# Kernel tuning notes

Measured on AMD Instinct MI355X. Metric: run time of the kernel, lower is better.

The kernel has to match this reference:

```python
import jax, jax.numpy as jnp
import numpy as np

# Gemma config constants (layer_idx=0 -> 'sliding_attention')
H = 8          # num query heads
KVH = 4        # num kv heads
DH = 256       # head_dim
SW = 1024      # sliding_window
ROPE_BASE = 10000.0   # rope_local_base_freq (sliding layer)
EPS = 1e-6
SCALE = 256.0 ** -0.5  # query_pre_attn_scalar ** -0.5


def _rms_norm(x, w):
    # Gemma RMSNorm: fp32 norm, scale by (1 + w)
    x32 = x.astype(jnp.float32)
    n = x32 * jax.lax.rsqrt(jnp.mean(x32 * x32, axis=-1, keepdims=True) + EPS)
    return (n * (1.0 + w.astype(jnp.float32))).astype(x.dtype)


def _rope_cos_sin(S):
    inv_freq = 1.0 / (ROPE_BASE ** (jnp.arange(0, DH, 2, dtype=jnp.float32) / DH))
    freqs = jnp.outer(jnp.arange(S, dtype=jnp.float32), inv_freq)  # [S, DH/2]
    emb = jnp.concatenate([freqs, freqs], axis=-1)                 # [S, DH]
    return jnp.cos(emb), jnp.sin(emb)


def _rotate_half(x):
    x1, x2 = jnp.split(x, 2, axis=-1)
    return jnp.concatenate([-x2, x1], axis=-1)


def _apply_rope(x, cos, sin):
    # x: [B, H, S, DH]; cos/sin: [S, DH]
    return x * cos[None, None] + _rotate_half(x) * sin[None, None]


def setup_inputs() -> dict:
    key = jax.random.key(0)
    ks = jax.random.split(key, 7)
    B, S, D = 2, 2048, 2048
    w = lambda k, shape: jax.random.normal(k, shape, jnp.float32) * 0.02
    return {
        "hidden_states": jax.random.normal(ks[0], (B, S, D), jnp.float32),
        "Wq": w(ks[1], (H * DH, D)),
        "Wk": w(ks[2], (KVH * DH, D)),
        "Wv": w(ks[3], (KVH * DH, D)),
        "Wo": w(ks[4], (D, H * DH)),
        "q_norm_w": jnp.zeros((DH,), jnp.float32),
        "k_norm_w": jnp.zeros((DH,), jnp.float32),
    }


def reference(hidden_states, Wq, Wk, Wv, Wo, q_norm_w, k_norm_w):
    B, S, D = hidden_states.shape
    # projections (no bias)
    q = jnp.einsum("bsd,ed->bse", hidden_states, Wq).reshape(B, S, H, DH).transpose(0, 2, 1, 3)
    k = jnp.einsum("bsd,ed->bse", hidden_states, Wk).reshape(B, S, KVH, DH).transpose(0, 2, 1, 3)
    v = jnp.einsum("bsd,ed->bse", hidden_states, Wv).reshape(B, S, KVH, DH).transpose(0, 2, 1, 3)
    # Gemma q/k RMSNorm over head_dim, then RoPE (local base for sliding layer)
    q = _rms_norm(q, q_norm_w)
    k = _rms_norm(k, k_norm_w)
    cos, sin = _rope_cos_sin(S)
    q = _apply_rope(q, cos, sin)
    k = _apply_rope(k, cos, sin)
    # GQA: repeat kv heads
    rep = H // KVH
    k = jnp.repeat(k, rep, axis=1)
    v = jnp.repeat(v, rep, axis=1)
    # causal sliding-window mask
    i = jnp.arange(S)[:, None]
    j = jnp.arange(S)[None, :]
    mask = (j <= i) & (i - j < SW)  # [S, S]
    scores = jnp.einsum("bhqd,bhkd->bhqk", q, k) * SCALE
    scores = jnp.where(mask[None, None], scores, jnp.finfo(jnp.float32).min)
    attn = jax.nn.softmax(scores.astype(jnp.float32), axis=-1).astype(q.dtype)
    out = jnp.einsum("bhqk,bhkd->bhqd", attn, v)  # [B, H, S, DH]
    out = out.transpose(0, 2, 1, 3).reshape(B, S, H * DH)
    return jnp.einsum("bse,de->bsd", out, Wo)
```

## Files before the change

### kernel.cpp

```cpp
#include <hip/hip_runtime.h>
#include <hip/hip_bf16.h>


typedef __bf16 bf16x8 __attribute__((ext_vector_type(8)));
typedef __bf16 bf16x4 __attribute__((ext_vector_type(4)));
typedef float f32x4 __attribute__((ext_vector_type(4)));

#define NB 2
#define SEQ 2048
#define DMODEL 2048
#define NH 8
#define NKV 4
#define DHEAD 256
#define SWIN 1024

#define AS1 __attribute__((address_space(1)))
#define AS3 __attribute__((address_space(3)))

static __device__ __forceinline__ void gload_lds16(const void* g, void* l) {
    __builtin_amdgcn_global_load_lds((const AS1 void*)g, (AS3 void*)l, 16, 0, 0);
}

static __device__ __forceinline__ bf16x4 tr16(const __bf16* p) {
    bf16x4 r;
    asm volatile("ds_read_b64_tr_b16 %0, %1" : "=v"(r) : "v"((const AS3 __bf16*)p));
    return r;
}

__global__ void cvt_rope(const float* __restrict__ s0, const float* __restrict__ s1,
                         const float* __restrict__ s2, const float* __restrict__ s3,
                         const float* __restrict__ s4, __bf16* __restrict__ d0,
                         __bf16* __restrict__ d1, __bf16* __restrict__ d2,
                         __bf16* __restrict__ d3, __bf16* __restrict__ d4,
                         float* __restrict__ cosT, float* __restrict__ sinT) {
    if (blockIdx.x >= 20480) {
        int idx = (blockIdx.x - 20480) * 256 + threadIdx.x;
        int s = idx >> 7, i = idx & 127;
        float fr = (float)s * __expf(-(float)i * 0.0719557843f);
        cosT[idx] = cosf(fr);
        sinT[idx] = sinf(fr);
        return;
    }
    int i = blockIdx.x * 256 + threadIdx.x;
    const float* src; __bf16* dst;
    if (i < 2097152) { src = s0; dst = d0; }
    else if (i < 3145728) { i -= 2097152; src = s1; dst = d1; }
    else if (i < 3670016) { i -= 3145728; src = s2; dst = d2; }
    else if (i < 4194304) { i -= 3670016; src = s3; dst = d3; }
    else                  { i -= 4194304; src = s4; dst = d4; }
    f32x4 v = ((const f32x4*)src)[i];
    bf16x4 o;
#pragma unroll
    for (int j = 0; j < 4; ++j) o[j] = (__bf16)v[j];
    ((bf16x4*)dst)[i] = o;
}

template <int OUTBF16>
__global__ __launch_bounds__(512, 2)
void gemm_bt8(const __bf16* __restrict__ A, const __bf16* __restrict__ B,
              void* __restrict__ Cv, int M, int N, int K, int nbx) {
    __shared__ __align__(16) __bf16 sA[2][256 * 64];
    __shared__ __align__(16) __bf16 sB[2][256 * 64];
    const int tid = threadIdx.x;
    const int wave = tid >> 6, lane = tid & 63;
    const int lo = lane & 15, hi = lane >> 4;
    const int wm = wave >> 2, wn = wave & 3;
    const int qq = (int)gridDim.x >> 3;
    const int swz = ((int)blockIdx.x & 7) * qq + ((int)blockIdx.x >> 3);
    const int bx = swz % nbx, by = swz / nbx;
    const int brow = by * 256, bcol = bx * 256;
    const int xr = lo & 7;

    int aoff[4];
#pragma unroll
    for (int i = 0; i < 4; ++i) {
        int n = i * 512 + tid, r = n >> 3, s = n & 7;
        aoff[i] = r * K + ((s ^ (r & 7)) << 3);
    }
    const __bf16* Ab = A + (size_t)brow * K;
    const __bf16* Bb = B + (size_t)bcol * K;

    auto stgA = [&](int bsel, int kt, int h) {
        const __bf16* ga = Ab + kt * 64;
#pragma unroll
        for (int ii = 0; ii < 2; ++ii) {
            int i = h + ii * 2;
            gload_lds16(ga + aoff[i], (char*)&sA[bsel][0] + (i * 512 + wave * 64) * 16);
        }
    };
    auto stgB = [&](int bsel, int kt, int h) {
        const __bf16* gb = Bb + kt * 64;
#pragma unroll
        for (int i = 2 * h; i < 2 * h + 2; ++i)
            gload_lds16(gb + aoff[i], (char*)&sB[bsel][0] + (i * 512 + wave * 64) * 16);
    };

    f32x4 acc[8][4] = {};
    const int nt = K >> 6;

    stgA(0, 0, 0); stgA(0, 0, 1); stgB(0, 0, 0); stgB(0, 0, 1);
    stgA(1, 1, 0); stgA(1, 1, 1); stgB(1, 1, 0); stgB(1, 1, 1);
    asm volatile("s_waitcnt vmcnt(8)" ::: "memory");
    __builtin_amdgcn_s_barrier();

    for (int t = 0; t < nt; ++t) {
        const int buf = t & 1;
        const bool pre = (t + 2 < nt);
        const __bf16* sa = &sA[buf][0];
        const __bf16* sb = &sB[buf][0];
        bf16x8 af[8], b0[4], b1[4];
#pragma unroll
        for (int m = 0; m < 4; ++m)
#pragma unroll
            for (int ks = 0; ks < 2; ++ks)
                af[m * 2 + ks] = *(const bf16x8*)&sa[(wm * 128 + m * 16 + lo) * 64 + (((ks * 4 + hi) ^ xr) << 3)];
#pragma unroll
        for (int n = 0; n < 2; ++n)
#pragma unroll
            for (int ks = 0; ks < 2; ++ks)
                b0[n * 2 + ks] = *(const bf16x8*)&sb[(wn * 64 + n * 16 + lo) * 64 + (((ks * 4 + hi) ^ xr) << 3)];
        __builtin_amdgcn_sched_barrier(0);
        __builtin_amdgcn_s_barrier();
        __builtin_amdgcn_s_setprio(1);
#pragma unroll
        for (int m = 0; m < 4; ++m)
#pragma unroll
            for (int n = 0; n < 2; ++n)
#pragma unroll
                for (int ks = 0; ks < 2; ++ks)
                    acc[m][n] = __builtin_amdgcn_mfma_f32_16x16x32_bf16(af[m * 2 + ks], b0[n * 2 + ks], acc[m][n], 0, 0, 0);
        __builtin_amdgcn_s_setprio(0);
        __builtin_amdgcn_sched_barrier(0);
        __builtin_amdgcn_s_barrier();
#pragma unroll
        for (int n = 0; n < 2; ++n)
#pragma unroll
            for (int ks = 0; ks < 2; ++ks)
                b1[n * 2 + ks] = *(const bf16x8*)&sb[(wn * 64 + (n + 2) * 16 + lo) * 64 + (((ks * 4 + hi) ^ xr) << 3)];
        if (pre) stgA(buf, t + 2, 0);
        __builtin_amdgcn_sched_barrier(0);
        __builtin_amdgcn_s_barrier();
        __builtin_amdgcn_s_setprio(1);
#pragma unroll
        for (int m = 0; m < 4; ++m)
#pragma unroll
            for (int n = 0; n < 2; ++n)
#pragma unroll
                for (int ks = 0; ks < 2; ++ks)
                    acc[m][n + 2] = __builtin_amdgcn_mfma_f32_16x16x32_bf16(af[m * 2 + ks], b1[n * 2 + ks], acc[m][n + 2], 0, 0, 0);
        __builtin_amdgcn_s_setprio(0);
        __builtin_amdgcn_sched_barrier(0);
        __builtin_amdgcn_s_barrier();
#pragma unroll
        for (int m = 0; m < 4; ++m)
#pragma unroll
            for (int ks = 0; ks < 2; ++ks)
                af[m * 2 + ks] = *(const bf16x8*)&sa[(wm * 128 + (m + 4) * 16 + lo) * 64 + (((ks * 4 + hi) ^ xr) << 3)];
        if (pre) stgB(buf, t + 2, 1);
        __builtin_amdgcn_sched_barrier(0);
        __builtin_amdgcn_s_barrier();
        __builtin_amdgcn_s_setprio(1);
#pragma unroll
        for (int m = 0; m < 4; ++m)
#pragma unroll
            for (int n = 0; n < 2; ++n)
#pragma unroll
                for (int ks = 0; ks < 2; ++ks)
                    acc[m + 4][n + 2] = __builtin_amdgcn_mfma_f32_16x16x32_bf16(af[m * 2 + ks], b1[n * 2 + ks], acc[m + 4][n + 2], 0, 0, 0);
        __builtin_amdgcn_s_setprio(0);
        __builtin_amdgcn_sched_barrier(0);
        __builtin_amdgcn_s_barrier();
        if (pre) { stgA(buf, t + 2, 1); stgB(buf, t + 2, 0); }
        __builtin_amdgcn_sched_barrier(0);
        __builtin_amdgcn_s_setprio(1);
#pragma unroll
        for (int m = 0; m < 4; ++m)
#pragma unroll
            for (int n = 0; n < 2; ++n)
#pragma unroll
                for (int ks = 0; ks < 2; ++ks)
                    acc[m + 4][n] = __builtin_amdgcn_mfma_f32_16x16x32_bf16(af[m * 2 + ks], b0[n * 2 + ks], acc[m + 4][n], 0, 0, 0);
        __builtin_amdgcn_s_setprio(0);
        if (pre) asm volatile("s_waitcnt vmcnt(8)" ::: "memory");
        else     asm volatile("s_waitcnt vmcnt(0)" ::: "memory");
        __builtin_amdgcn_sched_barrier(0);
        __builtin_amdgcn_s_barrier();
    }

#pragma unroll
    for (int m = 0; m < 8; ++m) {
        int row = brow + wm * 128 + m * 16 + hi * 4;
#pragma unroll
        for (int n = 0; n < 4; ++n) {
            int col = bcol + wn * 64 + n * 16 + lo;
            if constexpr (OUTBF16) {
                __bf16* cp = (__bf16*)Cv + (size_t)row * N + col;
#pragma unroll
                for (int j = 0; j < 4; ++j)
                    cp[(size_t)j * N] = (__bf16)acc[m][n][j];
            } else {
                float* cp = (float*)Cv + (size_t)row * N + col;
#pragma unroll
                for (int j = 0; j < 4; ++j)
                    cp[(size_t)j * N] = acc[m][n][j];
            }
        }
    }
}

__global__ __launch_bounds__(512, 2)
void gemm_bt8n(const __bf16* __restrict__ A, const __bf16* __restrict__ B,
               float* __restrict__ C, int M, int N, int K, int nbx) {
    __shared__ __align__(16) __bf16 sA[2][256 * 64];
    __shared__ __align__(16) __bf16 sB[2][128 * 64];
    const int tid = threadIdx.x;
    const int wave = tid >> 6, lane = tid & 63;
    const int lo = lane & 15, hi = lane >> 4;
    const int wm = wave >> 1, wn = wave & 1;
    const int qq = (int)gridDim.x >> 3;
    const int swz = ((int)blockIdx.x & 7) * qq + ((int)blockIdx.x >> 3);
    const int bx = swz % nbx, by = swz / nbx;
    const int brow = by * 256, bcol = bx * 128;
    const int xr = lo & 7;

    int aoff[4], boff[2];
#pragma unroll
    for (int i = 0; i < 4; ++i) {
        int n = i * 512 + tid, r = n >> 3, s = n & 7;
        aoff[i] = r * K + ((s ^ (r & 7)) << 3);
    }
#pragma unroll
    for (int i = 0; i < 2; ++i) {
        int n = i * 512 + tid, r = n >> 3, s = n & 7;
        boff[i] = r * K + ((s ^ (r & 7)) << 3);
    }
    const __bf16* Ab = A + (size_t)brow * K;
    const __bf16* Bb = B + (size_t)bcol * K;

    auto stgAall = [&](int bsel, int kt) {
        const __bf16* ga = Ab + kt * 64;
#pragma unroll
        for (int i = 0; i < 4; ++i)
            gload_lds16(ga + aoff[i], (char*)&sA[bsel][0] + (i * 512 + wave * 64) * 16);
    };
    auto stgBall = [&](int bsel, int kt) {
        const __bf16* gb = Bb + kt * 64;
#pragma unroll
        for (int i = 0; i < 2; ++i)
            gload_lds16(gb + boff[i], (char*)&sB[bsel][0] + (i * 512 + wave * 64) * 16);
    };

    f32x4 acc[4][4] = {};
    const int nt = K >> 6;

    stgAall(0, 0); stgBall(0, 0);
    stgAall(1, 1); stgBall(1, 1);
    asm volatile("s_waitcnt vmcnt(6)" ::: "memory");
    __builtin_amdgcn_s_barrier();

    for (int t = 0; t < nt; ++t) {
        const int buf = t & 1;
        const bool pre = (t + 2 < nt);
        const __bf16* sa = &sA[buf][0];
        const __bf16* sb = &sB[buf][0];
        bf16x8 af[4], b0[4], b1[4];
#pragma unroll
        for (int m = 0; m < 2; ++m)
#pragma unroll
            for (int ks = 0; ks < 2; ++ks)
                af[m * 2 + ks] = *(const bf16x8*)&sa[(wm * 64 + m * 16 + lo) * 64 + (((ks * 4 + hi) ^ xr) << 3)];
#pragma unroll
        for (int n = 0; n < 2; ++n)
#pragma unroll
            for (int ks = 0; ks < 2; ++ks)
                b0[n * 2 + ks] = *(const bf16x8*)&sb[(wn * 64 + n * 16 + lo) * 64 + (((ks * 4 + hi) ^ xr) << 3)];
        __builtin_amdgcn_sched_barrier(0);
        __builtin_amdgcn_s_barrier();
        __builtin_amdgcn_s_setprio(1);
#pragma unroll
        for (int m = 0; m < 2; ++m)
#pragma unroll
            for (int n = 0; n < 2; ++n)
#pragma unroll
                for (int ks = 0; ks < 2; ++ks)
                    acc[m][n] = __builtin_amdgcn_mfma_f32_16x16x32_bf16(af[m * 2 + ks], b0[n * 2 + ks], acc[m][n], 0, 0, 0);
        __builtin_amdgcn_s_setprio(0);
        __builtin_amdgcn_sched_barrier(0);
        __builtin_amdgcn_s_barrier();
#pragma unroll
        for (int n = 0; n < 2; ++n)
#pragma unroll
            for (int ks = 0; ks < 2; ++ks)
                b1[n * 2 + ks] = *(const bf16x8*)&sb[(wn * 64 + (n + 2) * 16 + lo) * 64 + (((ks * 4 + hi) ^ xr) << 3)];
        __builtin_amdgcn_sched_barrier(0);
        __builtin_amdgcn_s_barrier();
        __builtin_amdgcn_s_setprio(1);
#pragma unroll
        for (int m = 0; m < 2; ++m)
#pragma unroll
            for (int n = 0; n < 2; ++n)
#pragma unroll
                for (int ks = 0; ks < 2; ++ks)
                    acc[m][n + 2] = __builtin_amdgcn_mfma_f32_16x16x32_bf16(af[m * 2 + ks], b1[n * 2 + ks], acc[m][n + 2], 0, 0, 0);
        __builtin_amdgcn_s_setprio(0);
        __builtin_amdgcn_sched_barrier(0);
        __builtin_amdgcn_s_barrier();
#pragma unroll
        for (int m = 0; m < 2; ++m)
#pragma unroll
            for (int ks = 0; ks < 2; ++ks)
                af[m * 2 + ks] = *(const bf16x8*)&sa[(wm * 64 + (m + 2) * 16 + lo) * 64 + (((ks * 4 + hi) ^ xr) << 3)];
        if (pre) stgBall(buf, t + 2);
        __builtin_amdgcn_sched_barrier(0);
        __builtin_amdgcn_s_barrier();
        __builtin_amdgcn_s_setprio(1);
#pragma unroll
        for (int m = 0; m < 2; ++m)
#pragma unroll
            for (int n = 0; n < 2; ++n)
#pragma unroll
                for (int ks = 0; ks < 2; ++ks)
                    acc[m + 2][n + 2] = __builtin_amdgcn_mfma_f32_16x16x32_bf16(af[m * 2 + ks], b1[n * 2 + ks], acc[m + 2][n + 2], 0, 0, 0);
        __builtin_amdgcn_s_setprio(0);
        __builtin_amdgcn_sched_barrier(0);
        __builtin_amdgcn_s_barrier();
        if (pre) stgAall(buf, t + 2);
        __builtin_amdgcn_sched_barrier(0);
        __builtin_amdgcn_s_setprio(1);
#pragma unroll
        for (int m = 0; m < 2; ++m)
#pragma unroll
            for (int n = 0; n < 2; ++n)
#pragma unroll
                for (int ks = 0; ks < 2; ++ks)
                    acc[m + 2][n] = __builtin_amdgcn_mfma_f32_16x16x32_bf16(af[m * 2 + ks], b0[n * 2 + ks], acc[m + 2][n], 0, 0, 0);
        __builtin_amdgcn_s_setprio(0);
        if (pre) asm volatile("s_waitcnt vmcnt(6)" ::: "memory");
        else     asm volatile("s_waitcnt vmcnt(0)" ::: "memory");
        __builtin_amdgcn_sched_barrier(0);
        __builtin_amdgcn_s_barrier();
    }

#pragma unroll
    for (int m = 0; m < 4; ++m) {
        int row = brow + wm * 64 + m * 16 + hi * 4;
#pragma unroll
        for (int n = 0; n < 4; ++n) {
            float* cp = C + (size_t)row * N + bcol + wn * 64 + n * 16 + lo;
#pragma unroll
            for (int j = 0; j < 4; ++j)
                cp[(size_t)j * N] = acc[m][n][j];
        }
    }
}

__global__ __launch_bounds__(256)
void norm_rope(const __bf16* __restrict__ QKV, const float* __restrict__ qw,
               const float* __restrict__ kw, const float* __restrict__ cosT,
               const float* __restrict__ sinT, __bf16* __restrict__ Qo,
               __bf16* __restrict__ Ko, __bf16* __restrict__ Vo) {
    const int r = blockIdx.x;
    const int b = r >> 11, s = r & (SEQ - 1);
    const int wave = threadIdx.x >> 6, lane = threadIdx.x & 63;
    f32x4 cos4 = *(const f32x4*)&cosT[s * 128 + (lane & 31) * 4];
    f32x4 sin4 = *(const f32x4*)&sinT[s * 128 + (lane & 31) * 4];
#pragma unroll
    for (int ii = 0; ii < 4; ++ii) {
        int hh = wave + ii * 4;
        if (hh < 12) {
            bool isq = hh < 8;
            int col0 = isq ? hh * DHEAD : DMODEL + (hh - 8) * DHEAD;
            const __bf16* src = QKV + (size_t)r * 4096 + col0;
            bf16x4 xb = *(const bf16x4*)&src[lane * 4];
            float x[4];
#pragma unroll
            for (int j = 0; j < 4; ++j) x[j] = (float)xb[j];
            float ss = x[0] * x[0] + x[1] * x[1] + x[2] * x[2] + x[3] * x[3];
#pragma unroll
            for (int d2 = 1; d2 < 64; d2 <<= 1) ss += __shfl_xor(ss, d2);
            float scale = rsqrtf(ss * (1.f / DHEAD) + 1e-6f);
            const float* wp = isq ? qw : kw;
            float nx[4];
#pragma unroll
            for (int j = 0; j < 4; ++j)
                nx[j] = x[j] * scale * (1.f + wp[lane * 4 + j]);
            bf16x4 ov;
#pragma unroll
            for (int j = 0; j < 4; ++j) {
                float other = __shfl_xor(nx[j], 32);
                float rot = (lane < 32) ? -other : other;
                float v = nx[j] * cos4[j] + rot * sin4[j];
                if (isq) v *= 0.0625f;
                ov[j] = (__bf16)v;
            }
            __bf16* dst = isq ? (Qo + ((size_t)(b * NH + hh) * SEQ + s) * DHEAD)
                              : (Ko + ((size_t)(b * NKV + (hh - 8)) * SEQ + s) * DHEAD);
            *(bf16x4*)&dst[lane * 4] = ov;
        } else {
            int vh = hh - 12;
            const __bf16* src = QKV + (size_t)r * 4096 + 3072 + vh * DHEAD;
            bf16x4 xb = *(const bf16x4*)&src[lane * 4];
            __bf16* dst = Vo + ((size_t)(b * NKV + vh) * SEQ + s) * DHEAD;
            *(bf16x4*)&dst[lane * 4] = xb;
        }
    }
}

__global__ __launch_bounds__(256)
void attn8(const __bf16* __restrict__ Q, const __bf16* __restrict__ Kb,
           const __bf16* __restrict__ Vb, __bf16* __restrict__ ctx) {
    const int bid = blockIdx.x;
    const int bk = bid & 7;
    const int qt = 63 - (bid >> 3);
    const int b = bk >> 2, kh = bk & 3;
    const int q0 = qt * 32;
    const int tid = threadIdx.x;
    const int wave = tid >> 6, lane = tid & 63;
    const int lo = lane & 15, hi = lane >> 4;
    const int hsel = wave >> 1, qsub = wave & 1;
    const int h = kh * 2 + hsel;
    const int qbase = q0 + qsub * 16;
    const int q = qbase + lo;

    __shared__ __align__(16) __bf16 kbuf[2][32 * 256];
    __shared__ __align__(16) __bf16 vbuf[32 * 256];

    const __bf16* Qp = Q + ((size_t)(b * NH + h) * SEQ + qbase) * DHEAD;
    const __bf16* Kp = Kb + (size_t)(b * NKV + kh) * SEQ * DHEAD;
    const __bf16* Vp = Vb + (size_t)(b * NKV + kh) * SEQ * DHEAD;

    int koff[4], voff[4];
#pragma unroll
    for (int i = 0; i < 4; ++i) {
        int n = i * 256 + tid;
        int r = n >> 5, c = n & 31;
        koff[i] = r * 256 + ((c ^ (r & 7)) << 3);
        int st = n >> 3, w = n & 7;
        int vk = (st & 7) * 4 + (w >> 1);
        int vd = (st >> 3) * 16 + (w & 1) * 8;
        voff[i] = vk * 256 + vd;
    }

    auto stageK = [&](int bsel, int c0) {
        const __bf16* kg = Kp + (size_t)c0 * DHEAD;
        char* kd = (char*)&kbuf[bsel][0] + wave * 1024;
#pragma unroll
        for (int i = 0; i < 4; ++i) gload_lds16(kg + koff[i], kd + i * 4096);
    };
    auto stageV = [&](int c0) {
        const __bf16* vg = Vp + (size_t)c0 * DHEAD;
        char* vd = (char*)&vbuf[0] + wave * 1024;
#pragma unroll
        for (int i = 0; i < 4; ++i) gload_lds16(vg + voff[i], vd + i * 4096);
    };

    bf16x8 qf[8];
#pragma unroll
    for (int dc = 0; dc < 8; ++dc)
        qf[dc] = *(const bf16x8*)(Qp + (size_t)lo * DHEAD + dc * 32 + hi * 8);

    f32x4 o[16] = {};
    float m = -3e38f, l = 0.f;

    int kstart = q0 - SWIN; if (kstart < 0) kstart = 0;
    const int nt = (q0 + 32 - kstart) >> 5;

    stageK(0, kstart);
    asm volatile("s_waitcnt vmcnt(0)" ::: "memory");
    int buf = 0;
    for (int t = 0; t < nt; ++t) {
        const int c0 = kstart + t * 32;
        const bool pre = (t + 1 < nt);
        stageV(c0);
        if (pre) stageK(buf ^ 1, c0 + 32);
        if (pre) asm volatile("s_waitcnt vmcnt(8)" ::: "memory");
        else     asm volatile("s_waitcnt vmcnt(4)" ::: "memory");
        __builtin_amdgcn_sched_barrier(0);
        __builtin_amdgcn_s_barrier();
        __builtin_amdgcn_sched_barrier(0);

        f32x4 sc0 = {}, sc1 = {};
        const __bf16* kb0 = &kbuf[buf][0];
        __builtin_amdgcn_s_setprio(1);
#pragma unroll
        for (int dc = 0; dc < 8; ++dc) {
            int u = dc * 4 + hi;
            bf16x8 kfa = *(const bf16x8*)&kb0[lo * 256 + ((u ^ (lo & 7)) << 3)];
            bf16x8 kfb = *(const bf16x8*)&kb0[(16 + lo) * 256 + ((u ^ ((16 + lo) & 7)) << 3)];
            sc0 = __builtin_amdgcn_mfma_f32_16x16x32_bf16(kfa, qf[dc], sc0, 0, 0, 0);
            sc1 = __builtin_amdgcn_mfma_f32_16x16x32_bf16(kfb, qf[dc], sc1, 0, 0, 0);
        }
        __builtin_amdgcn_s_setprio(0);

        float s8[8];
#pragma unroll
        for (int j = 0; j < 4; ++j) {
            int ka = c0 + hi * 4 + j;
            int kb2 = ka + 16;
            s8[j]     = (ka <= q && q - ka < SWIN) ? sc0[j] : -1e30f;
            s8[4 + j] = (kb2 <= q && q - kb2 < SWIN) ? sc1[j] : -1e30f;
        }
        float pm = s8[0];
#pragma unroll
        for (int i = 1; i < 8; ++i) pm = fmaxf(pm, s8[i]);
        pm = fmaxf(pm, __shfl_xor(pm, 16));
        pm = fmaxf(pm, __shfl_xor(pm, 32));
        if (__any(pm > m + 8.f)) {
            float mn = fmaxf(m, pm);
            float corr = __expf(m - mn);
            l *= corr;
#pragma unroll
            for (int dt = 0; dt < 16; ++dt) o[dt] *= corr;
            m = mn;
        }
        float p8[8], ps = 0.f;
#pragma unroll
        for (int i = 0; i < 8; ++i) {
            float e = __expf(s8[i] - m);
            p8[i] = (s8[i] > -9e29f) ? e : 0.f;
            ps += p8[i];
        }
        ps += __shfl_xor(ps, 16);
        ps += __shfl_xor(ps, 32);
        l += ps;

        bf16x8 paf;
#pragma unroll
        for (int i = 0; i < 8; ++i) paf[i] = (__bf16)p8[i];

        if (pre) asm volatile("s_waitcnt vmcnt(4)" ::: "memory");
        else     asm volatile("s_waitcnt vmcnt(0)" ::: "memory");
        __builtin_amdgcn_sched_barrier(0);
        __builtin_amdgcn_s_barrier();
        __builtin_amdgcn_sched_barrier(0);

        const __bf16* vb0 = &vbuf[0];
        bf16x4 t0[16], t1[16];
#pragma unroll
        for (int dq = 0; dq < 4; ++dq) {
#pragma unroll
            for (int u = 0; u < 4; ++u) {
                int dt = dq * 4 + u;
                t0[dt] = tr16(vb0 + (dt * 8 + hi) * 64 + lo * 4);
                t1[dt] = tr16(vb0 + (dt * 8 + 4 + hi) * 64 + lo * 4);
            }
            __builtin_amdgcn_sched_barrier(0);
        }
#pragma unroll
        for (int dq = 0; dq < 4; ++dq) {
            if (dq == 0)      asm volatile("s_waitcnt lgkmcnt(15)" ::: "memory");
            else if (dq == 1) asm volatile("s_waitcnt lgkmcnt(15)" ::: "memory");
            else if (dq == 2) asm volatile("s_waitcnt lgkmcnt(8)"  ::: "memory");
            else              asm volatile("s_waitcnt lgkmcnt(0)"  ::: "memory");
            __builtin_amdgcn_sched_barrier(0);
            __builtin_amdgcn_s_setprio(1);
#pragma unroll
            for (int u = 0; u < 4; ++u) {
                int dt = dq * 4 + u;
                bf16x8 vf;
#pragma unroll
                for (int j = 0; j < 4; ++j) { vf[j] = t0[dt][j]; vf[4 + j] = t1[dt][j]; }
                o[dt] = __builtin_amdgcn_mfma_f32_16x16x32_bf16(vf, paf, o[dt], 0, 0, 0);
            }
            __builtin_amdgcn_s_setprio(0);
        }
        __builtin_amdgcn_sched_barrier(0);
        __builtin_amdgcn_s_barrier();
        __builtin_amdgcn_sched_barrier(0);
        buf ^= 1;
    }

    const float invl = 1.0f / l;
    __bf16* cp = ctx + ((size_t)(b * SEQ + q)) * (NH * DHEAD) + h * DHEAD;
#pragma unroll
    for (int dt = 0; dt < 16; ++dt) {
        bf16x4 w;
#pragma unroll
        for (int j = 0; j < 4; ++j) w[j] = (__bf16)(o[dt][j] * invl);
        *(bf16x4*)&cp[dt * 16 + hi * 4] = w;
    }
}

extern "C" void kernel_launch(void* const* d_in, const int* in_sizes, int n_in,
                              void* d_out, int out_size, void* d_ws, size_t ws_size,
                              hipStream_t stream) {
    const float* hs = (const float*)d_in[0];
    const float* Wq = (const float*)d_in[1];
    const float* Wk = (const float*)d_in[2];
    const float* Wv = (const float*)d_in[3];
    const float* Wo = (const float*)d_in[4];
    const float* qw = (const float*)d_in[5];
    const float* kw = (const float*)d_in[6];
    float* out = (float*)d_out;

    char* ws = (char*)d_ws;
    size_t off = 0;
    auto alloc = [&](size_t bytes) {
        char* p = ws + off;
        off += (bytes + 255) & ~(size_t)255;
        return p;
    };
    const int M = NB * SEQ;
    __bf16* hsB   = (__bf16*)alloc((size_t)M * DMODEL * 2);
    __bf16* WqkvB = (__bf16*)alloc((size_t)4096 * DMODEL * 2);
    __bf16* WoB   = (__bf16*)alloc((size_t)DMODEL * DMODEL * 2);
    __bf16* QKVb  = (__bf16*)alloc((size_t)M * 4096 * 2);
    __bf16* Qb    = (__bf16*)alloc((size_t)M * 2048 * 2);
    __bf16* Kbf   = (__bf16*)alloc((size_t)M * 1024 * 2);
    __bf16* Vbf   = (__bf16*)alloc((size_t)M * 1024 * 2);
    float*  cosT  = (float*) alloc((size_t)SEQ * 128 * 4);
    float*  sinT  = (float*) alloc((size_t)SEQ * 128 * 4);
    __bf16* ctxB  = QKVb;

    cvt_rope<<<21504, 256, 0, stream>>>(hs, Wq, Wk, Wv, Wo,
                                        hsB, WqkvB, WqkvB + (size_t)2048 * 2048,
                                        WqkvB + (size_t)3072 * 2048, WoB, cosT, sinT);

    gemm_bt8<1><<<256, 512, 0, stream>>>(hsB, WqkvB, QKVb, M, 4096, DMODEL, 16);

    norm_rope<<<M, 256, 0, stream>>>(QKVb, qw, kw, cosT, sinT, Qb, Kbf, Vbf);

    attn8<<<512, 256, 0, stream>>>(Qb, Kbf, Vbf, ctxB);

    gemm_bt8n<<<256, 512, 0, stream>>>(ctxB, WoB, out, M, DMODEL, DMODEL, 16);
}
```

Baseline: 204.7 us.

## Fuse q/k RMSNorm and RoPE epilogue into QKV projection GEMM

```diff
diff --git a/kernel.cpp b/kernel.cpp
--- a/kernel.cpp
+++ b/kernel.cpp
@@ -55,12 +55,13 @@
     ((bf16x4*)dst)[i] = o;
 }
 
-template <int OUTBF16>
 __global__ __launch_bounds__(512, 2)
-void gemm_bt8(const __bf16* __restrict__ A, const __bf16* __restrict__ B,
-              void* __restrict__ Cv, int M, int N, int K, int nbx) {
-    __shared__ __align__(16) __bf16 sA[2][256 * 64];
-    __shared__ __align__(16) __bf16 sB[2][256 * 64];
+void gemm_qkv(const __bf16* __restrict__ A, const __bf16* __restrict__ B,
+              const float* __restrict__ qw, const float* __restrict__ kw,
+              const float* __restrict__ cosT, const float* __restrict__ sinT,
+              __bf16* __restrict__ Qo, __bf16* __restrict__ Ko,
+              __bf16* __restrict__ Vo, int M, int N, int K, int nbx) {
+    __shared__ __align__(16) __bf16 smem[67584];
     const int tid = threadIdx.x;
     const int wave = tid >> 6, lane = tid & 63;
     const int lo = lane & 15, hi = lane >> 4;
@@ -68,7 +69,7 @@
     const int qq = (int)gridDim.x >> 3;
     const int swz = ((int)blockIdx.x & 7) * qq + ((int)blockIdx.x >> 3);
     const int bx = swz % nbx, by = swz / nbx;
-    const int brow = by * 256, bcol = bx * 256;
+    const int brow = by * 256;
     const int xr = lo & 7;
 
     int aoff[4];
@@ -78,21 +79,21 @@
         aoff[i] = r * K + ((s ^ (r & 7)) << 3);
     }
     const __bf16* Ab = A + (size_t)brow * K;
-    const __bf16* Bb = B + (size_t)bcol * K;
+    const __bf16* Bb = B + (size_t)(bx * 256) * K;
 
     auto stgA = [&](int bsel, int kt, int h) {
         const __bf16* ga = Ab + kt * 64;
 #pragma unroll
         for (int ii = 0; ii < 2; ++ii) {
             int i = h + ii * 2;
-            gload_lds16(ga + aoff[i], (char*)&sA[bsel][0] + (i * 512 + wave * 64) * 16);
+            gload_lds16(ga + aoff[i], (char*)(smem + bsel * 16384) + (i * 512 + wave * 64) * 16);
         }
     };
     auto stgB = [&](int bsel, int kt, int h) {
         const __bf16* gb = Bb + kt * 64;
 #pragma unroll
         for (int i = 2 * h; i < 2 * h + 2; ++i)
-            gload_lds16(gb + aoff[i], (char*)&sB[bsel][0] + (i * 512 + wave * 64) * 16);
+            gload_lds16(gb + aoff[i], (char*)(smem + 32768 + bsel * 16384) + (i * 512 + wave * 64) * 16);
     };
 
     f32x4 acc[8][4] = {};
@@ -106,8 +107,8 @@
     for (int t = 0; t < nt; ++t) {
         const int buf = t & 1;
         const bool pre = (t + 2 < nt);
-        const __bf16* sa = &sA[buf][0];
-        const __bf16* sb = &sB[buf][0];
+        const __bf16* sa = smem + buf * 16384;
+        const __bf16* sb = smem + 32768 + buf * 16384;
         bf16x8 af[8], b0[4], b1[4];
 #pragma unroll
         for (int m = 0; m < 4; ++m)
@@ -187,23 +188,64 @@
         __builtin_amdgcn_s_barrier();
     }
 
-#pragma unroll
-    for (int m = 0; m < 8; ++m) {
-        int row = brow + wm * 128 + m * 16 + hi * 4;
-#pragma unroll
-        for (int n = 0; n < 4; ++n) {
-            int col = bcol + wn * 64 + n * 16 + lo;
-            if constexpr (OUTBF16) {
-                __bf16* cp = (__bf16*)Cv + (size_t)row * N + col;
+    __syncthreads();
+    {
+#pragma unroll
+        for (int m = 0; m < 8; ++m)
+#pragma unroll
+            for (int n = 0; n < 4; ++n) {
+                int lr = wm * 128 + m * 16 + hi * 4;
+                int lc = wn * 64 + n * 16 + lo;
 #pragma unroll
                 for (int j = 0; j < 4; ++j)
-                    cp[(size_t)j * N] = (__bf16)acc[m][n][j];
+                    smem[(lr + j) * 264 + lc] = (__bf16)acc[m][n][j];
+            }
+        __syncthreads();
+
+        const bool isq = bx < 8;
+        const bool isv = bx >= 12;
+        float w4[4];
+        if (!isv) {
+            const float* wp = isq ? qw : kw;
+#pragma unroll
+            for (int j = 0; j < 4; ++j) w4[j] = 1.f + wp[lane * 4 + j];
+        }
+        __bf16* hbase = isq ? Qo : (isv ? Vo : Ko);
+        const int hidx = isq ? bx : (isv ? bx - 12 : bx - 8);
+        const int nheads = isq ? NH : NKV;
+
+        for (int rr = 0; rr < 32; ++rr) {
+            int lr = wave * 32 + rr;
+            int gs = brow + lr;
+            int bb = gs >> 11, s = gs & (SEQ - 1);
+            bf16x4 xb = *(const bf16x4*)&smem[lr * 264 + lane * 4];
+            bf16x4 ov;
+            if (isv) {
+                ov = xb;
             } else {
-                float* cp = (float*)Cv + (size_t)row * N + col;
-#pragma unroll
-                for (int j = 0; j < 4; ++j)
-                    cp[(size_t)j * N] = acc[m][n][j];
+                float x[4];
+#pragma unroll
+                for (int j = 0; j < 4; ++j) x[j] = (float)xb[j];
+                float ss = x[0] * x[0] + x[1] * x[1] + x[2] * x[2] + x[3] * x[3];
+#pragma unroll
+                for (int d2 = 1; d2 < 64; d2 <<= 1) ss += __shfl_xor(ss, d2);
+                float scale = rsqrtf(ss * (1.f / DHEAD) + 1e-6f);
+                float nx[4];
+#pragma unroll
+                for (int j = 0; j < 4; ++j) nx[j] = x[j] * scale * w4[j];
+                f32x4 cos4 = *(const f32x4*)&cosT[s * 128 + (lane & 31) * 4];
+                f32x4 sin4 = *(const f32x4*)&sinT[s * 128 + (lane & 31) * 4];
+#pragma unroll
+                for (int j = 0; j < 4; ++j) {
+                    float other = __shfl_xor(nx[j], 32);
+                    float rot = (lane < 32) ? -other : other;
+                    float v = nx[j] * cos4[j] + rot * sin4[j];
+                    if (isq) v *= 0.0625f;
+                    ov[j] = (__bf16)v;
+                }
             }
+            __bf16* dst = hbase + ((size_t)(bb * nheads + hidx) * SEQ + s) * DHEAD;
+            *(bf16x4*)&dst[lane * 4] = ov;
         }
     }
 }
@@ -350,58 +392,6 @@
 #pragma unroll
             for (int j = 0; j < 4; ++j)
                 cp[(size_t)j * N] = acc[m][n][j];
-        }
-    }
-}
-
-__global__ __launch_bounds__(256)
-void norm_rope(const __bf16* __restrict__ QKV, const float* __restrict__ qw,
-               const float* __restrict__ kw, const float* __restrict__ cosT,
-               const float* __restrict__ sinT, __bf16* __restrict__ Qo,
-               __bf16* __restrict__ Ko, __bf16* __restrict__ Vo) {
-    const int r = blockIdx.x;
-    const int b = r >> 11, s = r & (SEQ - 1);
-    const int wave = threadIdx.x >> 6, lane = threadIdx.x & 63;
-    f32x4 cos4 = *(const f32x4*)&cosT[s * 128 + (lane & 31) * 4];
-    f32x4 sin4 = *(const f32x4*)&sinT[s * 128 + (lane & 31) * 4];
-#pragma unroll
-    for (int ii = 0; ii < 4; ++ii) {
-        int hh = wave + ii * 4;
-        if (hh < 12) {
-            bool isq = hh < 8;
-            int col0 = isq ? hh * DHEAD : DMODEL + (hh - 8) * DHEAD;
-            const __bf16* src = QKV + (size_t)r * 4096 + col0;
-            bf16x4 xb = *(const bf16x4*)&src[lane * 4];
-            float x[4];
-#pragma unroll
-            for (int j = 0; j < 4; ++j) x[j] = (float)xb[j];
-            float ss = x[0] * x[0] + x[1] * x[1] + x[2] * x[2] + x[3] * x[3];
-#pragma unroll
-            for (int d2 = 1; d2 < 64; d2 <<= 1) ss += __shfl_xor(ss, d2);
-            float scale = rsqrtf(ss * (1.f / DHEAD) + 1e-6f);
-            const float* wp = isq ? qw : kw;
-            float nx[4];
-#pragma unroll
-            for (int j = 0; j < 4; ++j)
-                nx[j] = x[j] * scale * (1.f + wp[lane * 4 + j]);
-            bf16x4 ov;
-#pragma unroll
-            for (int j = 0; j < 4; ++j) {
-                float other = __shfl_xor(nx[j], 32);
-                float rot = (lane < 32) ? -other : other;
-                float v = nx[j] * cos4[j] + rot * sin4[j];
-                if (isq) v *= 0.0625f;
-                ov[j] = (__bf16)v;
-            }
-            __bf16* dst = isq ? (Qo + ((size_t)(b * NH + hh) * SEQ + s) * DHEAD)
-                              : (Ko + ((size_t)(b * NKV + (hh - 8)) * SEQ + s) * DHEAD);
-            *(bf16x4*)&dst[lane * 4] = ov;
-        } else {
-            int vh = hh - 12;
-            const __bf16* src = QKV + (size_t)r * 4096 + 3072 + vh * DHEAD;
-            bf16x4 xb = *(const bf16x4*)&src[lane * 4];
-            __bf16* dst = Vo + ((size_t)(b * NKV + vh) * SEQ + s) * DHEAD;
-            *(bf16x4*)&dst[lane * 4] = xb;
         }
     }
 }
@@ -604,21 +594,19 @@
     __bf16* hsB   = (__bf16*)alloc((size_t)M * DMODEL * 2);
     __bf16* WqkvB = (__bf16*)alloc((size_t)4096 * DMODEL * 2);
     __bf16* WoB   = (__bf16*)alloc((size_t)DMODEL * DMODEL * 2);
-    __bf16* QKVb  = (__bf16*)alloc((size_t)M * 4096 * 2);
     __bf16* Qb    = (__bf16*)alloc((size_t)M * 2048 * 2);
     __bf16* Kbf   = (__bf16*)alloc((size_t)M * 1024 * 2);
     __bf16* Vbf   = (__bf16*)alloc((size_t)M * 1024 * 2);
+    __bf16* ctxB  = (__bf16*)alloc((size_t)M * 2048 * 2);
     float*  cosT  = (float*) alloc((size_t)SEQ * 128 * 4);
     float*  sinT  = (float*) alloc((size_t)SEQ * 128 * 4);
-    __bf16* ctxB  = QKVb;
 
     cvt_rope<<<21504, 256, 0, stream>>>(hs, Wq, Wk, Wv, Wo,
                                         hsB, WqkvB, WqkvB + (size_t)2048 * 2048,
                                         WqkvB + (size_t)3072 * 2048, WoB, cosT, sinT);
 
-    gemm_bt8<1><<<256, 512, 0, stream>>>(hsB, WqkvB, QKVb, M, 4096, DMODEL, 16);
-
-    norm_rope<<<M, 256, 0, stream>>>(QKVb, qw, kw, cosT, sinT, Qb, Kbf, Vbf);
+    gemm_qkv<<<256, 512, 0, stream>>>(hsB, WqkvB, qw, kw, cosT, sinT,
+                                      Qb, Kbf, Vbf, M, 4096, DMODEL, 16);
 
     attn8<<<512, 256, 0, stream>>>(Qb, Kbf, Vbf, ctxB);
 
```

New measurement: 198.2 us. 1.03x faster.
